# Performance work log

Hardware: AMD Instinct MI355X
Metric: run time of the kernel (lower is better)

## Reference

```python
import jax, jax.numpy as jnp
import numpy as np

BN_EPS = 1e-5


def setup_inputs() -> dict:
    key = jax.random.key(0)
    ks = jax.random.split(key, 5)
    num = 65536
    x = jax.random.normal(ks[0], (num, 3, 256), dtype=jnp.float32)
    w1a = jax.random.normal(ks[1], (256, 768), dtype=jnp.float32) * (1.0 / np.sqrt(256))
    w2a = jax.random.normal(ks[2], (256, 768), dtype=jnp.float32) * (1.0 / np.sqrt(256))
    w1b = jax.random.normal(ks[3], (768, 768), dtype=jnp.float32) * (1.0 / np.sqrt(768))
    w2b = jax.random.normal(ks[4], (768, 768), dtype=jnp.float32) * (1.0 / np.sqrt(768))
    gamma = jnp.ones((768,), dtype=jnp.float32)
    beta = jnp.zeros((768,), dtype=jnp.float32)
    return {"x": x, "w1a": w1a, "w2a": w2a, "w1b": w1b, "w2b": w2b,
            "gamma": gamma, "beta": beta, "num": num}


def _sage_layer(h, w1, w2):
    # h: [num, 3, d_in]. For each hop, neighbors = mean of the other 2 hops
    # = (sum_over_hops - self) / 2. Then self @ w2 + neigh @ w1 (no activation,
    # matching the source which defines ReLU but never applies it).
    neigh = (h.sum(axis=1, keepdims=True) - h) * 0.5          # [num, 3, d_in]
    return jnp.einsum('nhd,de->nhe', h, w2) + jnp.einsum('nhd,de->nhe', neigh, w1)


def reference(x, w1a, w2a, w1b, w2b, gamma, beta, num):
    h = _sage_layer(x, w1a, w2a)      # [num, 3, 768]
    h = _sage_layer(h, w1b, w2b)      # [num, 3, 768]
    out = h[:, 0, :]                  # take hop 0 per graph item -> [num, 768]
    # BatchNorm1d(768), training mode: biased batch stats over the num axis
    mean = out.mean(axis=0)
    var = out.var(axis=0)             # ddof=0, matches torch normalization
    out = (out - mean) * jax.lax.rsqrt(var + BN_EPS) * gamma + beta
    return jax.nn.sigmoid(out)
```

## Files before the change

kernel.cpp:

```cpp
#include <hip/hip_runtime.h>
#include <cstdint>
#include <cstddef>

#define NSAMP 65536
#define KDIM  512
#define MDIM  768

typedef __attribute__((ext_vector_type(8))) _Float16 f16x8;
typedef __attribute__((ext_vector_type(4))) float f32x4;

union H2U { _Float16 h; unsigned short u; };
__device__ __forceinline__ unsigned short f2h(float f) {
  H2U v; v.h = (_Float16)f; return v.u;
}
__device__ __forceinline__ float h2f(unsigned short u) {
  H2U v; v.u = u; return (float)v.h;
}

__global__ __launch_bounds__(256) void prep_A_kernel(const float* __restrict__ x,
                                                     unsigned short* __restrict__ A) {
  int gid = blockIdx.x * 256 + threadIdx.x;
  int n  = gid >> 6;
  int cg = gid & 63;
  const float4* xr = (const float4*)(x + (size_t)n * 768);
  float4 a = xr[cg];
  float4 b = xr[64 + cg];
  float4 c = xr[128 + cg];
  ushort4 lo, hi;
  lo.x = f2h(a.x); lo.y = f2h(a.y); lo.z = f2h(a.z); lo.w = f2h(a.w);
  hi.x = f2h(a.x + b.x + c.x); hi.y = f2h(a.y + b.y + c.y);
  hi.z = f2h(a.z + b.z + c.z); hi.w = f2h(a.w + b.w + c.w);
  unsigned short* Arow = A + (size_t)n * KDIM;
  *(ushort4*)(Arow + cg * 4) = lo;
  *(ushort4*)(Arow + 256 + cg * 4) = hi;
}

__global__ __launch_bounds__(256) void prep_B_partial(const float* __restrict__ w1a,
                                                      const float* __restrict__ w2a,
                                                      const float* __restrict__ w1b,
                                                      const float* __restrict__ w2b,
                                                      float* __restrict__ temp) {
  int b = blockIdx.x;
  int jc = b & 3;
  int rem = b >> 2;
  int mc = rem % 3;
  int ic = rem / 3;
  int t = threadIdx.x;
  int m = mc * 256 + t;
  int i0 = ic * 8;
  int j0 = jc * 192;
  __shared__ __align__(16) float sC[8][192];
  __shared__ __align__(16) float s1[8][192];
  __shared__ __align__(16) float s2[8][192];
  for (int idx = t; idx < 8 * 192; idx += 256) {
    int ii = idx / 192, jj = idx % 192;
    float a1 = w1a[(size_t)(i0 + ii) * 768 + j0 + jj];
    float a2 = w2a[(size_t)(i0 + ii) * 768 + j0 + jj];
    s1[ii][jj] = a1; s2[ii][jj] = a2; sC[ii][jj] = a2 - 0.5f * a1;
  }
  __syncthreads();
  float acc1[8] = {0,0,0,0,0,0,0,0};
  float acc2[8] = {0,0,0,0,0,0,0,0};
  const float* pb1 = w1b + (size_t)j0 * 768 + m;
  const float* pb2 = w2b + (size_t)j0 * 768 + m;
  for (int jb = 0; jb < 192; jb += 4) {
    float F[4], Gp[4], Hh[4];
#pragma unroll
    for (int u = 0; u < 4; ++u) {
      float b1 = pb1[(size_t)(jb + u) * 768];
      float b2 = pb2[(size_t)(jb + u) * 768];
      F[u]  = b2 - 0.5f * b1;
      Gp[u] = 0.5f * b2 + 0.25f * b1;
      Hh[u] = 0.5f * b1;
    }
#pragma unroll
    for (int ii = 0; ii < 8; ++ii) {
      f32x4 c  = *(const f32x4*)&sC[ii][jb];
      f32x4 a1 = *(const f32x4*)&s1[ii][jb];
      f32x4 a2 = *(const f32x4*)&s2[ii][jb];
#pragma unroll
      for (int u = 0; u < 4; ++u) {
        acc1[ii] += c[u] * F[u];
        acc2[ii] += a1[u] * Gp[u] + a2[u] * Hh[u];
      }
    }
  }
  float* t1 = temp + ((size_t)jc * 768 + m) * 256 + i0;
  float* t2 = temp + ((size_t)(4 + jc) * 768 + m) * 256 + i0;
#pragma unroll
  for (int ii = 0; ii < 8; ++ii) { t1[ii] = acc1[ii]; t2[ii] = acc2[ii]; }
}

__global__ __launch_bounds__(256) void prep_B_convert(const float* __restrict__ temp,
                                                      unsigned short* __restrict__ Bt,
                                                      float* __restrict__ stats) {
  int idx = blockIdx.x * 256 + threadIdx.x;
  int i = idx & 255;
  int m = idx >> 8;
  const float* t1 = temp + (size_t)m * 256 + i;
  const float* t2 = temp + ((size_t)4 * 768 + m) * 256 + i;
  float v1 = 0.f, v2 = 0.f;
#pragma unroll
  for (int jc = 0; jc < 4; ++jc) {
    v1 += t1[(size_t)jc * 768 * 256];
    v2 += t2[(size_t)jc * 768 * 256];
  }
  Bt[(size_t)m * KDIM + i]       = f2h(v1);
  Bt[(size_t)m * KDIM + 256 + i] = f2h(v2);
  if (idx < 1536) stats[idx] = 0.f;
}

template <bool F16OUT>
__global__ __launch_bounds__(256) void gemm_kernel(const unsigned short* __restrict__ A,
                                                   const unsigned short* __restrict__ Bt,
                                                   float* __restrict__ outf,
                                                   unsigned short* __restrict__ outh,
                                                   float* __restrict__ stats) {
  __shared__ __align__(16) unsigned short As[128 * 32];
  __shared__ __align__(16) unsigned short Bs[128 * 32];

  int bid = blockIdx.x;
  int bm  = bid % 6;
  int bn  = bid / 6;
  int tid  = threadIdx.x;
  int wid  = tid >> 6;
  int lane = tid & 63;
  int quad = lane >> 4;
  int l15  = lane & 15;
  int wave_r = wid >> 1;
  int wave_c = wid & 1;

  size_t row0 = (size_t)bn * 128;
  int    col0 = bm * 128;

  f32x4 acc[4][4];
#pragma unroll
  for (int i = 0; i < 4; ++i)
#pragma unroll
    for (int j = 0; j < 4; ++j) acc[i][j] = (f32x4)(0.f);

  int chunk = lane & 3;
  int rsub  = lane >> 2;

  for (int k0 = 0; k0 < KDIM; k0 += 32) {
#pragma unroll
    for (int i = 0; i < 2; ++i) {
      int r = wid * 32 + i * 16 + rsub;
      const unsigned short* gA = A  + (row0 + r) * KDIM + k0 + chunk * 8;
      const unsigned short* gB = Bt + (size_t)(col0 + r) * KDIM + k0 + chunk * 8;
      unsigned short* lA = As + (wid * 32 + i * 16) * 32;
      unsigned short* lB = Bs + (wid * 32 + i * 16) * 32;
      __builtin_amdgcn_global_load_lds(
          (const __attribute__((address_space(1))) void*)(uintptr_t)gA,
          (__attribute__((address_space(3))) void*)(uint32_t)(uintptr_t)lA, 16, 0, 0);
      __builtin_amdgcn_global_load_lds(
          (const __attribute__((address_space(1))) void*)(uintptr_t)gB,
          (__attribute__((address_space(3))) void*)(uint32_t)(uintptr_t)lB, 16, 0, 0);
    }
    __syncthreads();

    f16x8 a[4], b[4];
#pragma unroll
    for (int rb = 0; rb < 4; ++rb)
      a[rb] = *(const f16x8*)&As[(wave_r * 64 + rb * 16 + l15) * 32 + quad * 8];
#pragma unroll
    for (int cb = 0; cb < 4; ++cb)
      b[cb] = *(const f16x8*)&Bs[(wave_c * 64 + cb * 16 + l15) * 32 + quad * 8];
#pragma unroll
    for (int rb = 0; rb < 4; ++rb)
#pragma unroll
      for (int cb = 0; cb < 4; ++cb)
        acc[rb][cb] = __builtin_amdgcn_mfma_f32_16x16x32_f16(a[rb], b[cb], acc[rb][cb], 0, 0, 0);
    __syncthreads();
  }

#pragma unroll
  for (int cb = 0; cb < 4; ++cb) {
    int col = col0 + wave_c * 64 + cb * 16 + l15;
    float s1 = 0.f, s2 = 0.f;
#pragma unroll
    for (int rb = 0; rb < 4; ++rb) {
      size_t rg = row0 + wave_r * 64 + rb * 16 + quad * 4;
#pragma unroll
      for (int reg = 0; reg < 4; ++reg) {
        float v = acc[rb][cb][reg];
        if (F16OUT) outh[(rg + reg) * MDIM + col] = f2h(v);
        else        outf[(rg + reg) * MDIM + col] = v;
        s1 += v;
        s2 += v * v;
      }
    }
    s1 += __shfl_xor(s1, 16); s1 += __shfl_xor(s1, 32);
    s2 += __shfl_xor(s2, 16); s2 += __shfl_xor(s2, 32);
    if (quad == 0) {
      atomicAdd(&stats[col], s1);
      atomicAdd(&stats[768 + col], s2);
    }
  }
}

__global__ void finalize_stats(const float* __restrict__ stats, const float* __restrict__ gamma,
                               const float* __restrict__ beta, float* __restrict__ ss) {
  int c = threadIdx.x;
  if (c < 768) {
    const float inv_n = 1.0f / 65536.0f;
    float mean = stats[c] * inv_n;
    float ex2  = stats[768 + c] * inv_n;
    float var  = ex2 - mean * mean;
    float scale = gamma[c] * rsqrtf(var + 1e-5f);
    ss[c]       = scale;
    ss[768 + c] = beta[c] - mean * scale;
  }
}

__global__ __launch_bounds__(256) void bn_sigmoid_h(const unsigned short* __restrict__ outpre,
                                                    const float* __restrict__ ss,
                                                    float* __restrict__ out) {
  int idx = blockIdx.x * 256 + threadIdx.x;
  int cg  = (idx % 96) * 8;
  f16x8 h = *(const f16x8*)(outpre + (size_t)idx * 8);
  float4 sc0 = *(const float4*)&ss[cg];
  float4 sc1 = *(const float4*)&ss[cg + 4];
  float4 sh0 = *(const float4*)&ss[768 + cg];
  float4 sh1 = *(const float4*)&ss[768 + cg + 4];
  float4 r0, r1;
  r0.x = 1.f / (1.f + __expf(-((float)h[0] * sc0.x + sh0.x)));
  r0.y = 1.f / (1.f + __expf(-((float)h[1] * sc0.y + sh0.y)));
  r0.z = 1.f / (1.f + __expf(-((float)h[2] * sc0.z + sh0.z)));
  r0.w = 1.f / (1.f + __expf(-((float)h[3] * sc0.w + sh0.w)));
  r1.x = 1.f / (1.f + __expf(-((float)h[4] * sc1.x + sh1.x)));
  r1.y = 1.f / (1.f + __expf(-((float)h[5] * sc1.y + sh1.y)));
  r1.z = 1.f / (1.f + __expf(-((float)h[6] * sc1.z + sh1.z)));
  r1.w = 1.f / (1.f + __expf(-((float)h[7] * sc1.w + sh1.w)));
  ((float4*)out)[(size_t)idx * 2]     = r0;
  ((float4*)out)[(size_t)idx * 2 + 1] = r1;
}

__global__ __launch_bounds__(256) void bn_sigmoid_f(float* __restrict__ out,
                                                    const float* __restrict__ ss) {
  int idx = blockIdx.x * 256 + threadIdx.x;
  int cg  = (idx % 192) * 4;
  float4 v  = ((const float4*)out)[idx];
  float4 sc = *(const float4*)&ss[cg];
  float4 sh = *(const float4*)&ss[768 + cg];
  v.x = 1.f / (1.f + __expf(-(v.x * sc.x + sh.x)));
  v.y = 1.f / (1.f + __expf(-(v.y * sc.y + sh.y)));
  v.z = 1.f / (1.f + __expf(-(v.z * sc.z + sh.z)));
  v.w = 1.f / (1.f + __expf(-(v.w * sc.w + sh.w)));
  ((float4*)out)[idx] = v;
}

extern "C" void kernel_launch(void* const* d_in, const int* in_sizes, int n_in,
                              void* d_out, int out_size, void* d_ws, size_t ws_size,
                              hipStream_t stream) {
  const float* x     = (const float*)d_in[0];
  const float* w1a   = (const float*)d_in[1];
  const float* w2a   = (const float*)d_in[2];
  const float* w1b   = (const float*)d_in[3];
  const float* w2b   = (const float*)d_in[4];
  const float* gamma = (const float*)d_in[5];
  const float* beta  = (const float*)d_in[6];
  float* out = (float*)d_out;

  size_t offA     = 0;
  size_t offBt    = offA + (size_t)NSAMP * KDIM * 2;
  size_t offTemp  = offBt + (size_t)MDIM * KDIM * 2;
  size_t offStats = offTemp + (size_t)2 * 4 * 768 * 256 * 4;
  size_t offSS    = offStats + 1536 * 4;
  size_t offOut   = (offSS + 1536 * 4 + 255) & ~(size_t)255;
  size_t needF16  = offOut + (size_t)NSAMP * MDIM * 2;

  unsigned short* A    = (unsigned short*)((char*)d_ws + offA);
  unsigned short* Bt   = (unsigned short*)((char*)d_ws + offBt);
  float* temp          = (float*)((char*)d_ws + offTemp);
  float* stats         = (float*)((char*)d_ws + offStats);
  float* ss            = (float*)((char*)d_ws + offSS);
  unsigned short* oh   = (unsigned short*)((char*)d_ws + offOut);
  bool f16stage = ws_size >= needF16;

  prep_A_kernel<<<NSAMP * 64 / 256, 256, 0, stream>>>(x, A);
  prep_B_partial<<<384, 256, 0, stream>>>(w1a, w2a, w1b, w2b, temp);
  prep_B_convert<<<768, 256, 0, stream>>>(temp, Bt, stats);
  if (f16stage) {
    gemm_kernel<true><<<(NSAMP / 128) * (MDIM / 128), 256, 0, stream>>>(A, Bt, nullptr, oh, stats);
    finalize_stats<<<1, 768, 0, stream>>>(stats, gamma, beta, ss);
    bn_sigmoid_h<<<(size_t)NSAMP * MDIM / 8 / 256, 256, 0, stream>>>(oh, ss, out);
  } else {
    gemm_kernel<false><<<(NSAMP / 128) * (MDIM / 128), 256, 0, stream>>>(A, Bt, out, nullptr, stats);
    finalize_stats<<<1, 768, 0, stream>>>(stats, gamma, beta, ss);
    bn_sigmoid_f<<<(size_t)NSAMP * MDIM / 4 / 256, 256, 0, stream>>>(out, ss);
  }
}
```

Before: 584.0 us.

## Double GEMM K-tile to 64 with XOR-swizzled LDS and grouped block order

The GEMM K-step grows from 32 to 64, which halves the number of barrier pairs per tile. LDS rows are stored with an XOR swizzle on the 16-byte chunk index so the fragment reads avoid bank conflicts. Block IDs are also remapped so that consecutive blocks spread across row tiles in groups of eight, meant to improve L2 locality. In exchange, LDS use doubles to 32KB per block, which may lower occupancy.

```diff
diff --git a/kernel.cpp b/kernel.cpp
--- a/kernel.cpp
+++ b/kernel.cpp
@@ -116,12 +116,13 @@
                                                    float* __restrict__ outf,
                                                    unsigned short* __restrict__ outh,
                                                    float* __restrict__ stats) {
-  __shared__ __align__(16) unsigned short As[128 * 32];
-  __shared__ __align__(16) unsigned short Bs[128 * 32];
+  __shared__ __align__(16) unsigned short As[128 * 64];
+  __shared__ __align__(16) unsigned short Bs[128 * 64];
 
   int bid = blockIdx.x;
-  int bm  = bid % 6;
-  int bn  = bid / 6;
+  int swz = (bid & 7) * 384 + (bid >> 3);
+  int bm  = swz % 6;
+  int bn  = swz / 6;
   int tid  = threadIdx.x;
   int wid  = tid >> 6;
   int lane = tid & 63;
@@ -139,17 +140,17 @@
 #pragma unroll
     for (int j = 0; j < 4; ++j) acc[i][j] = (f32x4)(0.f);
 
-  int chunk = lane & 3;
-  int rsub  = lane >> 2;
-
-  for (int k0 = 0; k0 < KDIM; k0 += 32) {
-#pragma unroll
-    for (int i = 0; i < 2; ++i) {
-      int r = wid * 32 + i * 16 + rsub;
-      const unsigned short* gA = A  + (row0 + r) * KDIM + k0 + chunk * 8;
-      const unsigned short* gB = Bt + (size_t)(col0 + r) * KDIM + k0 + chunk * 8;
-      unsigned short* lA = As + (wid * 32 + i * 16) * 32;
-      unsigned short* lB = Bs + (wid * 32 + i * 16) * 32;
+  int rsub = lane >> 3;
+  int ssw  = (lane & 7) ^ rsub;
+
+  for (int k0 = 0; k0 < KDIM; k0 += 64) {
+#pragma unroll
+    for (int i = 0; i < 4; ++i) {
+      int rl = i * 32 + wid * 8;
+      const unsigned short* gA = A  + (row0 + rl + rsub) * KDIM + k0 + ssw * 8;
+      const unsigned short* gB = Bt + (size_t)(col0 + rl + rsub) * KDIM + k0 + ssw * 8;
+      unsigned short* lA = As + rl * 64;
+      unsigned short* lB = Bs + rl * 64;
       __builtin_amdgcn_global_load_lds(
           (const __attribute__((address_space(1))) void*)(uintptr_t)gA,
           (__attribute__((address_space(3))) void*)(uint32_t)(uintptr_t)lA, 16, 0, 0);
@@ -159,18 +160,27 @@
     }
     __syncthreads();
 
-    f16x8 a[4], b[4];
-#pragma unroll
-    for (int rb = 0; rb < 4; ++rb)
-      a[rb] = *(const f16x8*)&As[(wave_r * 64 + rb * 16 + l15) * 32 + quad * 8];
-#pragma unroll
-    for (int cb = 0; cb < 4; ++cb)
-      b[cb] = *(const f16x8*)&Bs[(wave_c * 64 + cb * 16 + l15) * 32 + quad * 8];
-#pragma unroll
-    for (int rb = 0; rb < 4; ++rb)
-#pragma unroll
-      for (int cb = 0; cb < 4; ++cb)
-        acc[rb][cb] = __builtin_amdgcn_mfma_f32_16x16x32_f16(a[rb], b[cb], acc[rb][cb], 0, 0, 0);
+#pragma unroll
+    for (int ks = 0; ks < 2; ++ks) {
+      f16x8 a[4], b[4];
+#pragma unroll
+      for (int rb = 0; rb < 4; ++rb) {
+        int r  = wave_r * 64 + rb * 16 + l15;
+        int sl = (ks * 4 + quad) ^ (l15 & 7);
+        a[rb] = *(const f16x8*)&As[r * 64 + sl * 8];
+      }
+#pragma unroll
+      for (int cb = 0; cb < 4; ++cb) {
+        int r  = wave_c * 64 + cb * 16 + l15;
+        int sl = (ks * 4 + quad) ^ (l15 & 7);
+        b[cb] = *(const f16x8*)&Bs[r * 64 + sl * 8];
+      }
+#pragma unroll
+      for (int rb = 0; rb < 4; ++rb)
+#pragma unroll
+        for (int cb = 0; cb < 4; ++cb)
+          acc[rb][cb] = __builtin_amdgcn_mfma_f32_16x16x32_f16(a[rb], b[cb], acc[rb][cb], 0, 0, 0);
+    }
     __syncthreads();
   }
 
```

New measurement: 581.7 us. About the same (-0.4%).

## Load GEMM fragments directly from global into registers with double buffering

Applied to the files above, without the earlier changes.

Removes LDS staging and both per-iteration barriers in the GEMM. Each wave now loads its MFMA fragments straight from global memory into two alternating register sets, so loads for the next K slice overlap the current MFMAs. A block-index swizzle remaps tiles so that consecutive block IDs spread across row tiles, aiming for better L2 reuse. In exchange, the two waves that share a row or column of the 128x128 tile both fetch it, which doubles global/L2 traffic, and the 16-byte strided row reads may coalesce poorly.

```diff
diff --git a/kernel.cpp b/kernel.cpp
--- a/kernel.cpp
+++ b/kernel.cpp
@@ -116,12 +116,10 @@
                                                    float* __restrict__ outf,
                                                    unsigned short* __restrict__ outh,
                                                    float* __restrict__ stats) {
-  __shared__ __align__(16) unsigned short As[128 * 32];
-  __shared__ __align__(16) unsigned short Bs[128 * 32];
-
   int bid = blockIdx.x;
-  int bm  = bid % 6;
-  int bn  = bid / 6;
+  int swz = (bid & 7) * 384 + (bid >> 3);
+  int bm  = swz % 6;
+  int bn  = swz / 6;
   int tid  = threadIdx.x;
   int wid  = tid >> 6;
   int lane = tid & 63;
@@ -139,40 +137,41 @@
 #pragma unroll
     for (int j = 0; j < 4; ++j) acc[i][j] = (f32x4)(0.f);
 
-  int chunk = lane & 3;
-  int rsub  = lane >> 2;
-
-  for (int k0 = 0; k0 < KDIM; k0 += 32) {
-#pragma unroll
-    for (int i = 0; i < 2; ++i) {
-      int r = wid * 32 + i * 16 + rsub;
-      const unsigned short* gA = A  + (row0 + r) * KDIM + k0 + chunk * 8;
-      const unsigned short* gB = Bt + (size_t)(col0 + r) * KDIM + k0 + chunk * 8;
-      unsigned short* lA = As + (wid * 32 + i * 16) * 32;
-      unsigned short* lB = Bs + (wid * 32 + i * 16) * 32;
-      __builtin_amdgcn_global_load_lds(
-          (const __attribute__((address_space(1))) void*)(uintptr_t)gA,
-          (__attribute__((address_space(3))) void*)(uint32_t)(uintptr_t)lA, 16, 0, 0);
-      __builtin_amdgcn_global_load_lds(
-          (const __attribute__((address_space(1))) void*)(uintptr_t)gB,
-          (__attribute__((address_space(3))) void*)(uint32_t)(uintptr_t)lB, 16, 0, 0);
-    }
-    __syncthreads();
-
-    f16x8 a[4], b[4];
-#pragma unroll
-    for (int rb = 0; rb < 4; ++rb)
-      a[rb] = *(const f16x8*)&As[(wave_r * 64 + rb * 16 + l15) * 32 + quad * 8];
-#pragma unroll
-    for (int cb = 0; cb < 4; ++cb)
-      b[cb] = *(const f16x8*)&Bs[(wave_c * 64 + cb * 16 + l15) * 32 + quad * 8];
-#pragma unroll
-    for (int rb = 0; rb < 4; ++rb)
-#pragma unroll
-      for (int cb = 0; cb < 4; ++cb)
-        acc[rb][cb] = __builtin_amdgcn_mfma_f32_16x16x32_f16(a[rb], b[cb], acc[rb][cb], 0, 0, 0);
-    __syncthreads();
-  }
+  const unsigned short* baseA = A  + (row0 + wave_r * 64 + l15) * KDIM + quad * 8;
+  const unsigned short* baseB = Bt + (size_t)(col0 + wave_c * 64 + l15) * KDIM + quad * 8;
+
+#define LOADSET(aF, bF, kk)                                                        \
+  do {                                                                             \
+    _Pragma("unroll")                                                              \
+    for (int rb = 0; rb < 4; ++rb)                                                 \
+      aF[rb] = *(const f16x8*)(baseA + (size_t)rb * (16 * KDIM) + (kk));           \
+    _Pragma("unroll")                                                              \
+    for (int cb = 0; cb < 4; ++cb)                                                 \
+      bF[cb] = *(const f16x8*)(baseB + (size_t)cb * (16 * KDIM) + (kk));           \
+  } while (0)
+
+#define MFMASET(aF, bF)                                                            \
+  do {                                                                             \
+    _Pragma("unroll")                                                              \
+    for (int rb = 0; rb < 4; ++rb)                                                 \
+      _Pragma("unroll")                                                            \
+      for (int cb = 0; cb < 4; ++cb)                                               \
+        acc[rb][cb] =                                                              \
+            __builtin_amdgcn_mfma_f32_16x16x32_f16(aF[rb], bF[cb], acc[rb][cb],    \
+                                                   0, 0, 0);                       \
+  } while (0)
+
+  f16x8 a0[4], b0[4], a1[4], b1[4];
+  LOADSET(a0, b0, 0);
+#pragma unroll
+  for (int k0 = 0; k0 < KDIM; k0 += 64) {
+    LOADSET(a1, b1, k0 + 32);
+    MFMASET(a0, b0);
+    if (k0 + 64 < KDIM) LOADSET(a0, b0, k0 + 64);
+    MFMASET(a1, b1);
+  }
+#undef LOADSET
+#undef MFMASET
 
 #pragma unroll
   for (int cb = 0; cb < 4; ++cb) {
```

New measurement: 662.5 us. 13.4% more time.
